# Kernel optimization log

Hardware: AMD Instinct MI355X
Metric: run time of the kernel (lower is better)

The kernel has to match this reference:

```python
import jax, jax.numpy as jnp
import numpy as np

T = 48  # top-T from init

def setup_inputs() -> dict:
    key = jax.random.key(0)
    ks = jax.random.split(key, 8)
    B, C, H, W = 16, 512, 32, 32
    tc = C // 8
    return {
        "x": jax.random.normal(ks[0], (B, C, H, W), jnp.float32),
        "fW": jax.random.normal(ks[1], (tc, C), jnp.float32) * 0.05,
        "fb": jax.random.normal(ks[2], (tc,), jnp.float32) * 0.05,
        "gW": jax.random.normal(ks[3], (tc, C), jnp.float32) * 0.05,
        "gb": jax.random.normal(ks[4], (tc,), jnp.float32) * 0.05,
        "hW": jax.random.normal(ks[5], (C, C), jnp.float32) * 0.05,
        "hb": jax.random.normal(ks[6], (C,), jnp.float32) * 0.05,
        "scale": jax.random.normal(ks[7], (1,), jnp.float32),
    }

def reference(x, fW, fb, gW, gb, hW, hb, scale):
    B, C, H, W = x.shape
    tc = fW.shape[0]
    HW = H * W
    # normalize by Frobenius norm over (batch, channel) -> [H, W]
    xn = x / jnp.linalg.norm(x, axis=(0, 1))[None, None]  # [B,C,H,W]
    # 1x1 convs, output already channel-last [B,H,W,out]
    f = jnp.einsum('bchw,oc->bhwo', xn, fW) + fb          # [B,H,W,tc]
    g = jnp.einsum('bchw,oc->bhwo', xn, gW) + gb          # [B,H,W,tc]
    h = jnp.einsum('bchw,oc->bhwo', xn, hW) + hb          # [B,H,W,C]
    xp = jnp.transpose(xn, (0, 2, 3, 1))                  # [B,H,W,C]
    # scores: queries H-major, keys W-major (faithful to permute(0,3,2,1).reshape)
    g_keys = jnp.transpose(g, (0, 3, 2, 1)).reshape(B, tc, HW)  # [B,tc,W*H]
    s = jnp.matmul(f.reshape(B, HW, tc), g_keys)          # [B,HW,HW]
    beta = jax.nn.softmax(s, axis=-1)
    o = jnp.matmul(beta, h.reshape(B, HW, C)).reshape(B, H, W, C)
    fdd = scale * o + xp                                  # [B,H,W,C]
    # per-batch correlation: fdd[b] ([H,W,C]) @ fdd[b].reshape(C,HW)
    corr = jnp.einsum('bhwc,bcn->bhwn', fdd, fdd.reshape(B, C, HW))  # [B,H,W,HW]
    top = jax.lax.top_k(corr, T)[0]                       # descending top-T values
    top = jax.nn.relu(top)
    top = top / jnp.linalg.norm(top, axis=(0, 1))[None, None]  # norm over (B,H) -> [W,T]
    return jnp.transpose(top, (0, 3, 1, 2))               # [B,T,H,W]
```

## Files before the change

### kernel.cpp

```cpp
#include <hip/hip_runtime.h>
#include <cstdint>
#include <cstddef>

#define B_   16
#define C_   512
#define H_   32
#define W_   32
#define HW_  1024
#define TC_  64
#define T_   48

typedef unsigned short u16;
typedef __attribute__((ext_vector_type(8))) short short8v;
typedef __attribute__((ext_vector_type(4))) float f32x4;

__device__ __forceinline__ u16 tobf(float x) {
    unsigned u = __float_as_uint(x);
    return (u16)((u + 0x7FFFu + ((u >> 16) & 1u)) >> 16);
}
__device__ __forceinline__ float frombf(u16 h) {
    return __uint_as_float(((unsigned)h) << 16);
}

__device__ __forceinline__ void gld16(const void* g, void* l) {
    __builtin_amdgcn_global_load_lds(
        (const __attribute__((address_space(1))) void*)g,
        (__attribute__((address_space(3))) void*)l, 16, 0, 0);
}

__global__ void k_colsq(const float* __restrict__ x, float* __restrict__ partial) {
    int bid = blockIdx.x;
    int col = (bid & 3) * 256 + threadIdx.x;
    int r0  = (bid >> 2) * 256;
    const float* p = x + (size_t)r0 * HW_ + col;
    float s = 0.f;
    for (int r = 0; r < 256; ++r) { float v = p[(size_t)r * HW_]; s += v * v; }
    partial[(size_t)(bid >> 2) * HW_ + col] = s;
}

__global__ void k_rsqrt(const float* __restrict__ partial, float* __restrict__ ninv) {
    int i = blockIdx.x * 256 + threadIdx.x;
    if (i < HW_) {
        float s = 0.f;
        for (int r = 0; r < 32; ++r) s += partial[(size_t)r * HW_ + i];
        ninv[i] = rsqrtf(s);
    }
}

__global__ void k_transpose(const float* __restrict__ x, const float* __restrict__ ninv,
                            u16* __restrict__ obH) {
    __shared__ float tile[32][33];
    int b  = blockIdx.z;
    int m0 = blockIdx.x * 32, c0 = blockIdx.y * 32;
    int tx = threadIdx.x, ty = threadIdx.y;
    const float* xb = x + (size_t)b * C_ * HW_;
    #pragma unroll
    for (int j = 0; j < 32; j += 8)
        tile[ty + j][tx] = xb[(size_t)(c0 + ty + j) * HW_ + m0 + tx];
    __syncthreads();
    size_t base = (size_t)b * HW_ * C_;
    #pragma unroll
    for (int j = 0; j < 32; j += 8) {
        int m = m0 + ty + j;
        obH[base + (size_t)m * C_ + c0 + tx] = tobf(tile[tx][ty + j] * ninv[m]);
    }
}

__global__ void k_packW(const float* __restrict__ in, u16* __restrict__ oh) {
    size_t i = (size_t)blockIdx.x * 256 + threadIdx.x;
    oh[i] = tobf(in[i]);
}
__global__ void k_packFG(const float* __restrict__ fW, const float* __restrict__ gW,
                         const float* __restrict__ fb, const float* __restrict__ gb,
                         u16* __restrict__ oh, float* __restrict__ fgb) {
    int idx = blockIdx.x * 256 + threadIdx.x;
    int row = idx >> 9, c = idx & 511;
    float v = (row < 64) ? fW[row * 512 + c] : gW[(row - 64) * 512 + c];
    oh[idx] = tobf(v);
    if (idx < 128) fgb[idx] = (idx < 64) ? fb[idx] : gb[idx - 64];
}

template<int PERMB, int EPI, int KU>
__global__ __launch_bounds__(256) void k_gemm1(
    const u16* __restrict__ A, const u16* __restrict__ Bm,
    const float* __restrict__ bias,
    float* __restrict__ Cf, u16* __restrict__ Ch,
    const float* __restrict__ scaleP,
    int N, int K, int lda, int ldb, long sA, long sB, long sC)
{
    __shared__ u16 lds[8192 * KU];
    const int b = blockIdx.z;
    const u16* pA = A + (size_t)b * sA;
    const u16* pB = Bm + (size_t)b * sB;
    const int m0 = blockIdx.y * 128, n0 = blockIdx.x * 128;
    const int tid = threadIdx.x, wave = tid >> 6, lane = tid & 63;
    const int wm = wave >> 1, wn = wave & 1;
    const int g = lane >> 4;

    f32x4 acc[4][4];
    #pragma unroll
    for (int i = 0; i < 4; ++i)
        #pragma unroll
        for (int j = 0; j < 4; ++j) { f32x4 z = {0.f,0.f,0.f,0.f}; acc[i][j] = z; }

    for (int kt = 0; kt < (K >> 5); kt += KU) {
        __syncthreads();
        #pragma unroll
        for (int u = 0; u < KU; ++u) {
            const int k0 = (kt + u) << 5;
            u16* lb = lds + u * 8192;
            #pragma unroll
            for (int q = 0; q < 4; ++q) {
                int ci = wave * 4 + q;
                bool isA = ci < 8;
                int li = ci & 7;
                const u16* gp = isA ? pA : pB;
                int ld = isA ? lda : ldb;
                int rb = isA ? m0 : n0;
                int rp = li * 8 + (lane >> 3);
                int gg = (lane & 7) ^ (rp & 7);
                int r  = rp * 2 + (gg >> 2);
                int kc = k0 + (gg & 3) * 8;
                int rowg = rb + r;
                if (PERMB && !isA) rowg = ((rowg & 31) << 5) | (rowg >> 5);
                gld16(gp + (size_t)rowg * ld + kc,
                      lb + (isA ? 0 : 4096) + li * 512 + lane * 8);
            }
        }
        __syncthreads();
        #pragma unroll
        for (int u = 0; u < KU; ++u) {
            const u16* As = lds + u * 8192;
            const u16* Bs = As + 4096;
            short8v av[4];
            #pragma unroll
            for (int i = 0; i < 4; ++i) {
                int r = wm * 64 + i * 16 + (lane & 15);
                int rp = r >> 1, gg = ((r & 1) << 2) + g;
                av[i] = *(const short8v*)(As + rp * 64 + ((gg ^ (rp & 7)) << 3));
            }
            #pragma unroll
            for (int j = 0; j < 4; ++j) {
                int r = wn * 64 + j * 16 + (lane & 15);
                int rp = r >> 1, gg = ((r & 1) << 2) + g;
                short8v bv = *(const short8v*)(Bs + rp * 64 + ((gg ^ (rp & 7)) << 3));
                #pragma unroll
                for (int i = 0; i < 4; ++i)
                    acc[i][j] = __builtin_amdgcn_mfma_f32_16x16x32_bf16(av[i], bv, acc[i][j], 0, 0, 0);
            }
        }
    }

    const float sc = (EPI == 2) ? scaleP[0] : 0.f;
    const int colbase = n0 + wn * 64 + (lane & 15);
    const int rowbase = m0 + wm * 64 + ((lane >> 4) << 2);
    #pragma unroll
    for (int i = 0; i < 4; ++i)
        #pragma unroll
        for (int j = 0; j < 4; ++j) {
            int col = colbase + j * 16;
            #pragma unroll
            for (int rg = 0; rg < 4; ++rg) {
                int row = rowbase + i * 16 + rg;
                size_t idx = (size_t)b * sC + (size_t)row * N + col;
                float a = acc[i][j][rg];
                if (EPI == 0)      Cf[idx] = a;
                else if (EPI == 2) Ch[idx] = tobf(sc * a + frombf(Ch[idx]));
                else if (EPI == 4) Ch[idx] = tobf(a);
                else if (EPI == 5) Ch[idx] = tobf(a + bias[row]);
                else               Ch[idx] = tobf(a + bias[col]);
            }
        }
}

template<int PERMB, int EPI, int KU>
__global__ __launch_bounds__(512) void k_gemm2(
    const u16* __restrict__ A, const u16* __restrict__ Bm,
    const float* __restrict__ bias,
    float* __restrict__ Cf, u16* __restrict__ Ch,
    const float* __restrict__ scaleP,
    int N, int K, int lda, int ldb, long sA, long sB, long sC)
{
    __shared__ u16 lds[12288 * KU];
    const int b = blockIdx.z;
    const u16* pA = A + (size_t)b * sA;
    const u16* pB = Bm + (size_t)b * sB;
    const int m0 = blockIdx.y * 128, n0 = blockIdx.x * 256;
    const int tid = threadIdx.x, wave = tid >> 6, lane = tid & 63;
    const int wm = wave >> 2, wn = wave & 3;
    const int g = lane >> 4;

    f32x4 acc[4][4];
    #pragma unroll
    for (int i = 0; i < 4; ++i)
        #pragma unroll
        for (int j = 0; j < 4; ++j) { f32x4 z = {0.f,0.f,0.f,0.f}; acc[i][j] = z; }

    for (int kt = 0; kt < (K >> 5); kt += KU) {
        __syncthreads();
        #pragma unroll
        for (int u = 0; u < KU; ++u) {
            const int k0 = (kt + u) << 5;
            u16* lb = lds + u * 12288;
            #pragma unroll
            for (int q = 0; q < 3; ++q) {
                int ci = wave * 3 + q;
                bool isA = ci < 8;
                int li = isA ? ci : ci - 8;
                const u16* gp = isA ? pA : pB;
                int ld = isA ? lda : ldb;
                int rb = isA ? m0 : n0;
                int rp = li * 8 + (lane >> 3);
                int gg = (lane & 7) ^ (rp & 7);
                int r  = rp * 2 + (gg >> 2);
                int kc = k0 + (gg & 3) * 8;
                int rowg = rb + r;
                if (PERMB && !isA) rowg = ((rowg & 31) << 5) | (rowg >> 5);
                gld16(gp + (size_t)rowg * ld + kc,
                      lb + (isA ? 0 : 4096) + li * 512 + lane * 8);
            }
        }
        __syncthreads();
        #pragma unroll
        for (int u = 0; u < KU; ++u) {
            const u16* As = lds + u * 12288;
            const u16* Bs = As + 4096;
            short8v av[4];
            #pragma unroll
            for (int i = 0; i < 4; ++i) {
                int r = wm * 64 + i * 16 + (lane & 15);
                int rp = r >> 1, gg = ((r & 1) << 2) + g;
                av[i] = *(const short8v*)(As + rp * 64 + ((gg ^ (rp & 7)) << 3));
            }
            #pragma unroll
            for (int j = 0; j < 4; ++j) {
                int r = wn * 64 + j * 16 + (lane & 15);
                int rp = r >> 1, gg = ((r & 1) << 2) + g;
                short8v bv = *(const short8v*)(Bs + rp * 64 + ((gg ^ (rp & 7)) << 3));
                #pragma unroll
                for (int i = 0; i < 4; ++i)
                    acc[i][j] = __builtin_amdgcn_mfma_f32_16x16x32_bf16(av[i], bv, acc[i][j], 0, 0, 0);
            }
        }
    }

    const float sc = (EPI == 2) ? scaleP[0] : 0.f;
    const int colbase = n0 + wn * 64 + (lane & 15);
    const int rowbase = m0 + wm * 64 + ((lane >> 4) << 2);
    #pragma unroll
    for (int i = 0; i < 4; ++i)
        #pragma unroll
        for (int j = 0; j < 4; ++j) {
            int col = colbase + j * 16;
            #pragma unroll
            for (int rg = 0; rg < 4; ++rg) {
                int row = rowbase + i * 16 + rg;
                size_t idx = (size_t)b * sC + (size_t)row * N + col;
                float a = acc[i][j][rg];
                if (EPI == 0)      Cf[idx] = a;
                else if (EPI == 2) Ch[idx] = tobf(sc * a + frombf(Ch[idx]));
                else if (EPI == 4) Ch[idx] = tobf(a);
                else if (EPI == 5) Ch[idx] = tobf(a + bias[row]);
                else               Ch[idx] = tobf(a + bias[col]);
            }
        }
}

__global__ __launch_bounds__(256) void k_softmax(u16* __restrict__ S) {
    size_t row = blockIdx.x;
    u16* r = S + row * (size_t)HW_;
    int t = threadIdx.x;
    ushort4 raw = ((const ushort4*)r)[t];
    float v0 = frombf(raw.x), v1 = frombf(raw.y), v2 = frombf(raw.z), v3 = frombf(raw.w);

    __shared__ float redm[4], reds[4];
    int wid = t >> 6, lane = t & 63;

    float m = fmaxf(fmaxf(v0, v1), fmaxf(v2, v3));
    for (int o = 32; o > 0; o >>= 1) m = fmaxf(m, __shfl_down(m, o));
    if (lane == 0) redm[wid] = m;
    __syncthreads();
    if (t == 0) redm[0] = fmaxf(fmaxf(redm[0], redm[1]), fmaxf(redm[2], redm[3]));
    __syncthreads();
    m = redm[0];

    v0 = expf(v0 - m); v1 = expf(v1 - m); v2 = expf(v2 - m); v3 = expf(v3 - m);
    float s = v0 + v1 + v2 + v3;
    for (int o = 32; o > 0; o >>= 1) s += __shfl_down(s, o);
    if (lane == 0) reds[wid] = s;
    __syncthreads();
    if (t == 0) reds[0] = reds[0] + reds[1] + reds[2] + reds[3];
    __syncthreads();
    float inv = 1.f / reds[0];
    ushort4 o4;
    o4.x = tobf(v0 * inv); o4.y = tobf(v1 * inv);
    o4.z = tobf(v2 * inv); o4.w = tobf(v3 * inv);
    ((ushort4*)r)[t] = o4;
}

__global__ void k_tposeU1(const u16* __restrict__ src, u16* __restrict__ dst) {
    __shared__ u16 tile[32][33];
    int b = blockIdx.z;
    const u16* sb = src + (size_t)b * (C_ * HW_);
    u16* db = dst + (size_t)b * (C_ * HW_);
    int c0 = blockIdx.x * 32, r0 = blockIdx.y * 32;
    int tx = threadIdx.x, ty = threadIdx.y;
    #pragma unroll
    for (int j = 0; j < 32; j += 8)
        tile[ty + j][tx] = sb[(size_t)(r0 + ty + j) * HW_ + c0 + tx];
    __syncthreads();
    #pragma unroll
    for (int j = 0; j < 32; j += 8)
        db[(size_t)(c0 + ty + j) * C_ + r0 + tx] = tile[tx][ty + j];
}

__device__ __forceinline__ float sort64_desc(float v, int lane) {
    #pragma unroll
    for (int k = 2; k <= 64; k <<= 1) {
        #pragma unroll
        for (int j = k >> 1; j > 0; j >>= 1) {
            float o = __shfl_xor(v, j);
            bool takeMax = (((lane & k) == 0) == ((lane & j) == 0));
            v = takeMax ? fmaxf(v, o) : fminf(v, o);
        }
    }
    return v;
}
__device__ __forceinline__ float bmerge64_desc(float a, float b, int lane) {
    float br = __shfl(b, 63 - lane);
    float c = fmaxf(a, br);
    #pragma unroll
    for (int j = 32; j > 0; j >>= 1) {
        float o = __shfl_xor(c, j);
        c = ((lane & j) == 0) ? fmaxf(c, o) : fminf(c, o);
    }
    return c;
}

__global__ __launch_bounds__(256) void k_topk(const float* __restrict__ corr,
                                              float* __restrict__ topv) {
    __shared__ float buf[4][1024];
    int wave = threadIdx.x >> 6, lane = threadIdx.x & 63;
    int row = blockIdx.x * 4 + wave;
    const float4* rp = (const float4*)(corr + (size_t)row * HW_);

    float4 e[4];
    #pragma unroll
    for (int q = 0; q < 4; ++q) e[q] = rp[lane * 4 + q];

    float gm = -INFINITY;
    #pragma unroll
    for (int q = 0; q < 4; ++q)
        gm = fmaxf(gm, fmaxf(fmaxf(e[q].x, e[q].y), fmaxf(e[q].z, e[q].w)));
    float sorted = sort64_desc(gm, lane);
    float tau = __shfl(sorted, T_ - 1);

    int c = 0;
    #pragma unroll
    for (int q = 0; q < 4; ++q)
        c += (e[q].x >= tau) + (e[q].y >= tau) + (e[q].z >= tau) + (e[q].w >= tau);
    int sc = c;
    #pragma unroll
    for (int o = 1; o < 64; o <<= 1) {
        int t2 = __shfl_up(sc, o);
        if (lane >= o) sc += t2;
    }
    int off = sc - c;
    int cnt = __shfl(sc, 63);

    float* wb = buf[wave];
    #pragma unroll
    for (int q = 0; q < 4; ++q) {
        if (e[q].x >= tau) wb[off++] = e[q].x;
        if (e[q].y >= tau) wb[off++] = e[q].y;
        if (e[q].z >= tau) wb[off++] = e[q].z;
        if (e[q].w >= tau) wb[off++] = e[q].w;
    }

    float* orow = topv + (size_t)row * T_;
    if (cnt <= 64) {
        float a = (lane < cnt) ? wb[lane] : -INFINITY;
        a = sort64_desc(a, lane);
        if (lane < T_) orow[lane] = fmaxf(a, 0.f);
    } else if (cnt <= 128) {
        float a  = sort64_desc(wb[lane], lane);
        float b2 = sort64_desc((lane < cnt - 64) ? wb[64 + lane] : -INFINITY, lane);
        float m2 = bmerge64_desc(a, b2, lane);
        if (lane < T_) orow[lane] = fmaxf(m2, 0.f);
    } else {
        int P = 256; while (P < cnt) P <<= 1;
        for (int i = cnt + lane; i < P; i += 64) wb[i] = -INFINITY;
        for (int k = 2; k <= P; k <<= 1)
            for (int j = k >> 1; j > 0; j >>= 1)
                for (int t2 = lane; t2 < P; t2 += 64) {
                    int ixj = t2 ^ j;
                    if (ixj > t2) {
                        float a = wb[t2], b3 = wb[ixj];
                        bool desc = ((t2 & k) == 0);
                        if (desc ? (a < b3) : (a > b3)) { wb[t2] = b3; wb[ixj] = a; }
                    }
                }
        if (lane < T_) orow[lane] = fmaxf(wb[lane], 0.f);
    }
}

__global__ void k_colss(const float* __restrict__ topv, float* __restrict__ colss) {
    int o = blockIdx.x;
    int w = o / T_, t = o % T_;
    int lane = threadIdx.x;
    float s = 0.f;
    for (int i = lane; i < 512; i += 64) {
        int b = i >> 5, h = i & 31;
        float v = topv[(size_t)((b << 10) + (h << 5) + w) * T_ + t];
        s += v * v;
    }
    for (int off = 32; off > 0; off >>= 1) s += __shfl_down(s, off);
    if (lane == 0) colss[o] = s;
}

__global__ void k_final(const float* __restrict__ topv, const float* __restrict__ colss,
                        float* __restrict__ out) {
    int idx = blockIdx.x * 256 + threadIdx.x;
    if (idx >= B_ * T_ * HW_) return;
    int w = idx & 31;
    int h = (idx >> 5) & 31;
    int t = (idx >> 10) % T_;
    int b = idx / (T_ * HW_);
    float v = topv[(size_t)((b << 10) + (h << 5) + w) * T_ + t];
    out[idx] = v * rsqrtf(colss[w * T_ + t]);
}

extern "C" void kernel_launch(void* const* d_in, const int* in_sizes, int n_in,
                              void* d_out, int out_size, void* d_ws, size_t ws_size,
                              hipStream_t stream) {
    const float* x     = (const float*)d_in[0];
    const float* fW    = (const float*)d_in[1];
    const float* fb    = (const float*)d_in[2];
    const float* gW    = (const float*)d_in[3];
    const float* gb    = (const float*)d_in[4];
    const float* hW    = (const float*)d_in[5];
    const float* hb    = (const float*)d_in[6];
    const float* scale = (const float*)d_in[7];
    float* out = (float*)d_out;

    char* wsb = (char*)d_ws;
    float* part = (float*)(wsb + 0);
    float* ninv = (float*)(wsb + 131072);
    u16*   hWh  = (u16*)(wsb + 135168);
    u16*   fgWh = (u16*)(wsb + 1183744);
    float* fgb  = (float*)(wsb + 1445888);
    u16*   xnH  = (u16*)(wsb + 1446400);
    u16*   fgH  = (u16*)(wsb + 35000832);
    u16*   fgL  = (u16*)(wsb + 39195136);
    u16*   hvTH = (u16*)(wsb + 43389440);
    float* S    = (float*)(wsb + 76943872);
    float* topv = (float*)fgH;
    float* colss= (float*)fgL;
    u16*   Sp   = (u16*)S;

    const long sXn = 524288;
    const long sFG = 131072;
    const long sS  = 1048576;

    k_colsq<<<128, 256, 0, stream>>>(x, part);
    k_rsqrt<<<4, 256, 0, stream>>>(part, ninv);

    k_transpose<<<dim3(32, 16, 16), dim3(32, 8), 0, stream>>>(x, ninv, xnH);

    k_packW<<<1024, 256, 0, stream>>>(hW, hWh);
    k_packFG<<<256, 256, 0, stream>>>(fW, gW, fb, gb, fgWh, fgb);

    k_gemm1<0, 6, 2><<<dim3(1, 8, 16), 256, 0, stream>>>(
        xnH, fgWh, fgb, nullptr, fgH, nullptr,
        128, 512, 512, 512, sXn, 0, sFG);

    k_gemm2<0, 5, 2><<<dim3(4, 4, 16), 512, 0, stream>>>(
        hWh, xnH, hb, nullptr, hvTH, nullptr,
        1024, 512, 512, 512, 0, sXn, sXn);

    k_gemm2<1, 4, 2><<<dim3(4, 8, 16), 512, 0, stream>>>(
        fgH, fgH + 64, nullptr, nullptr, Sp, nullptr,
        1024, 64, 128, 128, sFG, sFG, sS);

    k_softmax<<<B_ * HW_, 256, 0, stream>>>(Sp);

    k_gemm2<0, 2, 2><<<dim3(2, 8, 16), 512, 0, stream>>>(
        Sp, hvTH, nullptr, nullptr, xnH, scale,
        512, 1024, 1024, 1024, sS, sXn, sXn);

    k_tposeU1<<<dim3(32, 16, 16), dim3(32, 8), 0, stream>>>(xnH, hvTH);

    k_gemm2<0, 0, 2><<<dim3(4, 8, 16), 512, 0, stream>>>(
        xnH, hvTH, nullptr, S, nullptr, nullptr,
        1024, 512, 512, 512, sXn, sXn, sS);

    k_topk<<<B_ * HW_ / 4, 256, 0, stream>>>(S, topv);

    k_colss<<<W_ * T_, 64, 0, stream>>>(topv, colss);
    k_final<<<(B_ * T_ * HW_ + 255) / 256, 256, 0, stream>>>(topv, colss, out);
}
```

Measured before the change: 220.4 us.

## Double-buffer GEMM LDS tiles to overlap global loads with MFMA compute

Replaces the KU=2 unrolled load-then-compute loop in both GEMM kernels with a ping-pong LDS pipeline. The next K-tile is issued with async global-to-LDS loads while the current tile is computed, using partial vmcnt waits and raw s_barrier plus sched_barrier fences. The goal is to hide global memory latency behind MFMA work. In exchange there are two barriers per 32-wide K step instead of one per 64, and correctness depends on the hand-set vmcnt counts matching the loads issued per stage.

```diff
diff --git a/kernel.cpp b/kernel.cpp
--- a/kernel.cpp
+++ b/kernel.cpp
@@ -80,7 +80,7 @@
     if (idx < 128) fgb[idx] = (idx < 64) ? fb[idx] : gb[idx - 64];
 }
 
-template<int PERMB, int EPI, int KU>
+template<int PERMB, int EPI>
 __global__ __launch_bounds__(256) void k_gemm1(
     const u16* __restrict__ A, const u16* __restrict__ Bm,
     const float* __restrict__ bias,
@@ -88,7 +88,7 @@
     const float* __restrict__ scaleP,
     int N, int K, int lda, int ldb, long sA, long sB, long sC)
 {
-    __shared__ u16 lds[8192 * KU];
+    __shared__ u16 lds[2 * 8192];
     const int b = blockIdx.z;
     const u16* pA = A + (size_t)b * sA;
     const u16* pB = Bm + (size_t)b * sB;
@@ -103,52 +103,64 @@
         #pragma unroll
         for (int j = 0; j < 4; ++j) { f32x4 z = {0.f,0.f,0.f,0.f}; acc[i][j] = z; }
 
-    for (int kt = 0; kt < (K >> 5); kt += KU) {
-        __syncthreads();
-        #pragma unroll
-        for (int u = 0; u < KU; ++u) {
-            const int k0 = (kt + u) << 5;
-            u16* lb = lds + u * 8192;
+    auto STAGE = [&](int kt, int half) {
+        const int k0 = kt << 5;
+        u16* lb = lds + half * 8192;
+        #pragma unroll
+        for (int q = 0; q < 4; ++q) {
+            int ci = wave * 4 + q;
+            bool isA = ci < 8;
+            int li = ci & 7;
+            const u16* gp = isA ? pA : pB;
+            int ld = isA ? lda : ldb;
+            int rb = isA ? m0 : n0;
+            int rp = li * 8 + (lane >> 3);
+            int gg = (lane & 7) ^ (rp & 7);
+            int r  = rp * 2 + (gg >> 2);
+            int kc = k0 + (gg & 3) * 8;
+            int rowg = rb + r;
+            if (PERMB && !isA) rowg = ((rowg & 31) << 5) | (rowg >> 5);
+            gld16(gp + (size_t)rowg * ld + kc,
+                  lb + (isA ? 0 : 4096) + li * 512 + lane * 8);
+        }
+    };
+    auto COMPUTE = [&](int half) {
+        const u16* As = lds + half * 8192;
+        const u16* Bs = As + 4096;
+        short8v av[4];
+        #pragma unroll
+        for (int i = 0; i < 4; ++i) {
+            int r = wm * 64 + i * 16 + (lane & 15);
+            int rp = r >> 1, gg = ((r & 1) << 2) + g;
+            av[i] = *(const short8v*)(As + rp * 64 + ((gg ^ (rp & 7)) << 3));
+        }
+        #pragma unroll
+        for (int j = 0; j < 4; ++j) {
+            int r = wn * 64 + j * 16 + (lane & 15);
+            int rp = r >> 1, gg = ((r & 1) << 2) + g;
+            short8v bv = *(const short8v*)(Bs + rp * 64 + ((gg ^ (rp & 7)) << 3));
             #pragma unroll
-            for (int q = 0; q < 4; ++q) {
-                int ci = wave * 4 + q;
-                bool isA = ci < 8;
-                int li = ci & 7;
-                const u16* gp = isA ? pA : pB;
-                int ld = isA ? lda : ldb;
-                int rb = isA ? m0 : n0;
-                int rp = li * 8 + (lane >> 3);
-                int gg = (lane & 7) ^ (rp & 7);
-                int r  = rp * 2 + (gg >> 2);
-                int kc = k0 + (gg & 3) * 8;
-                int rowg = rb + r;
-                if (PERMB && !isA) rowg = ((rowg & 31) << 5) | (rowg >> 5);
-                gld16(gp + (size_t)rowg * ld + kc,
-                      lb + (isA ? 0 : 4096) + li * 512 + lane * 8);
-            }
-        }
-        __syncthreads();
-        #pragma unroll
-        for (int u = 0; u < KU; ++u) {
-            const u16* As = lds + u * 8192;
-            const u16* Bs = As + 4096;
-            short8v av[4];
-            #pragma unroll
-            for (int i = 0; i < 4; ++i) {
-                int r = wm * 64 + i * 16 + (lane & 15);
-                int rp = r >> 1, gg = ((r & 1) << 2) + g;
-                av[i] = *(const short8v*)(As + rp * 64 + ((gg ^ (rp & 7)) << 3));
-            }
-            #pragma unroll
-            for (int j = 0; j < 4; ++j) {
-                int r = wn * 64 + j * 16 + (lane & 15);
-                int rp = r >> 1, gg = ((r & 1) << 2) + g;
-                short8v bv = *(const short8v*)(Bs + rp * 64 + ((gg ^ (rp & 7)) << 3));
-                #pragma unroll
-                for (int i = 0; i < 4; ++i)
-                    acc[i][j] = __builtin_amdgcn_mfma_f32_16x16x32_bf16(av[i], bv, acc[i][j], 0, 0, 0);
-            }
-        }
+            for (int i = 0; i < 4; ++i)
+                acc[i][j] = __builtin_amdgcn_mfma_f32_16x16x32_bf16(av[i], bv, acc[i][j], 0, 0, 0);
+        }
+    };
+
+    const int nkt = K >> 5;
+    STAGE(0, 0);
+    int cur = 0;
+    for (int kt = 0; kt < nkt; ++kt) {
+        if (kt + 1 < nkt) {
+            STAGE(kt + 1, cur ^ 1);
+            asm volatile("s_waitcnt vmcnt(4)" ::: "memory");
+        } else {
+            asm volatile("s_waitcnt vmcnt(0)" ::: "memory");
+        }
+        __builtin_amdgcn_s_barrier();
+        __builtin_amdgcn_sched_barrier(0);
+        COMPUTE(cur);
+        __builtin_amdgcn_sched_barrier(0);
+        __builtin_amdgcn_s_barrier();
+        cur ^= 1;
     }
 
     const float sc = (EPI == 2) ? scaleP[0] : 0.f;
@@ -173,7 +185,7 @@
         }
 }
 
-template<int PERMB, int EPI, int KU>
+template<int PERMB, int EPI>
 __global__ __launch_bounds__(512) void k_gemm2(
     const u16* __restrict__ A, const u16* __restrict__ Bm,
     const float* __restrict__ bias,
@@ -181,7 +193,7 @@
     const float* __restrict__ scaleP,
     int N, int K, int lda, int ldb, long sA, long sB, long sC)
 {
-    __shared__ u16 lds[12288 * KU];
+    __shared__ u16 lds[2 * 12288];
     const int b = blockIdx.z;
     const u16* pA = A + (size_t)b * sA;
     const u16* pB = Bm + (size_t)b * sB;
@@ -196,52 +208,64 @@
         #pragma unroll
         for (int j = 0; j < 4; ++j) { f32x4 z = {0.f,0.f,0.f,0.f}; acc[i][j] = z; }
 
-    for (int kt = 0; kt < (K >> 5); kt += KU) {
-        __syncthreads();
-        #pragma unroll
-        for (int u = 0; u < KU; ++u) {
-            const int k0 = (kt + u) << 5;
-            u16* lb = lds + u * 12288;
+    auto STAGE = [&](int kt, int half) {
+        const int k0 = kt << 5;
+        u16* lb = lds + half * 12288;
+        #pragma unroll
+        for (int q = 0; q < 3; ++q) {
+            int ci = wave * 3 + q;
+            bool isA = ci < 8;
+            int li = isA ? ci : ci - 8;
+            const u16* gp = isA ? pA : pB;
+            int ld = isA ? lda : ldb;
+            int rb = isA ? m0 : n0;
+            int rp = li * 8 + (lane >> 3);
+            int gg = (lane & 7) ^ (rp & 7);
+            int r  = rp * 2 + (gg >> 2);
+            int kc = k0 + (gg & 3) * 8;
+            int rowg = rb + r;
+            if (PERMB && !isA) rowg = ((rowg & 31) << 5) | (rowg >> 5);
+            gld16(gp + (size_t)rowg * ld + kc,
+                  lb + (isA ? 0 : 4096) + li * 512 + lane * 8);
+        }
+    };
+    auto COMPUTE = [&](int half) {
+        const u16* As = lds + half * 12288;
+        const u16* Bs = As + 4096;
+        short8v av[4];
+        #pragma unroll
+        for (int i = 0; i < 4; ++i) {
+            int r = wm * 64 + i * 16 + (lane & 15);
+            int rp = r >> 1, gg = ((r & 1) << 2) + g;
+            av[i] = *(const short8v*)(As + rp * 64 + ((gg ^ (rp & 7)) << 3));
+        }
+        #pragma unroll
+        for (int j = 0; j < 4; ++j) {
+            int r = wn * 64 + j * 16 + (lane & 15);
+            int rp = r >> 1, gg = ((r & 1) << 2) + g;
+            short8v bv = *(const short8v*)(Bs + rp * 64 + ((gg ^ (rp & 7)) << 3));
             #pragma unroll
-            for (int q = 0; q < 3; ++q) {
-                int ci = wave * 3 + q;
-                bool isA = ci < 8;
-                int li = isA ? ci : ci - 8;
-                const u16* gp = isA ? pA : pB;
-                int ld = isA ? lda : ldb;
-                int rb = isA ? m0 : n0;
-                int rp = li * 8 + (lane >> 3);
-                int gg = (lane & 7) ^ (rp & 7);
-                int r  = rp * 2 + (gg >> 2);
-                int kc = k0 + (gg & 3) * 8;
-                int rowg = rb + r;
-                if (PERMB && !isA) rowg = ((rowg & 31) << 5) | (rowg >> 5);
-                gld16(gp + (size_t)rowg * ld + kc,
-                      lb + (isA ? 0 : 4096) + li * 512 + lane * 8);
-            }
-        }
-        __syncthreads();
-        #pragma unroll
-        for (int u = 0; u < KU; ++u) {
-            const u16* As = lds + u * 12288;
-            const u16* Bs = As + 4096;
-            short8v av[4];
-            #pragma unroll
-            for (int i = 0; i < 4; ++i) {
-                int r = wm * 64 + i * 16 + (lane & 15);
-                int rp = r >> 1, gg = ((r & 1) << 2) + g;
-                av[i] = *(const short8v*)(As + rp * 64 + ((gg ^ (rp & 7)) << 3));
-            }
-            #pragma unroll
-            for (int j = 0; j < 4; ++j) {
-                int r = wn * 64 + j * 16 + (lane & 15);
-                int rp = r >> 1, gg = ((r & 1) << 2) + g;
-                short8v bv = *(const short8v*)(Bs + rp * 64 + ((gg ^ (rp & 7)) << 3));
-                #pragma unroll
-                for (int i = 0; i < 4; ++i)
-                    acc[i][j] = __builtin_amdgcn_mfma_f32_16x16x32_bf16(av[i], bv, acc[i][j], 0, 0, 0);
-            }
-        }
+            for (int i = 0; i < 4; ++i)
+                acc[i][j] = __builtin_amdgcn_mfma_f32_16x16x32_bf16(av[i], bv, acc[i][j], 0, 0, 0);
+        }
+    };
+
+    const int nkt = K >> 5;
+    STAGE(0, 0);
+    int cur = 0;
+    for (int kt = 0; kt < nkt; ++kt) {
+        if (kt + 1 < nkt) {
+            STAGE(kt + 1, cur ^ 1);
+            asm volatile("s_waitcnt vmcnt(3)" ::: "memory");
+        } else {
+            asm volatile("s_waitcnt vmcnt(0)" ::: "memory");
+        }
+        __builtin_amdgcn_s_barrier();
+        __builtin_amdgcn_sched_barrier(0);
+        COMPUTE(cur);
+        __builtin_amdgcn_sched_barrier(0);
+        __builtin_amdgcn_s_barrier();
+        cur ^= 1;
     }
 
     const float sc = (EPI == 2) ? scaleP[0] : 0.f;
@@ -470,27 +494,27 @@
     k_packW<<<1024, 256, 0, stream>>>(hW, hWh);
     k_packFG<<<256, 256, 0, stream>>>(fW, gW, fb, gb, fgWh, fgb);
 
-    k_gemm1<0, 6, 2><<<dim3(1, 8, 16), 256, 0, stream>>>(
+    k_gemm1<0, 6><<<dim3(1, 8, 16), 256, 0, stream>>>(
         xnH, fgWh, fgb, nullptr, fgH, nullptr,
         128, 512, 512, 512, sXn, 0, sFG);
 
-    k_gemm2<0, 5, 2><<<dim3(4, 4, 16), 512, 0, stream>>>(
+    k_gemm2<0, 5><<<dim3(4, 4, 16), 512, 0, stream>>>(
         hWh, xnH, hb, nullptr, hvTH, nullptr,
         1024, 512, 512, 512, 0, sXn, sXn);
 
-    k_gemm2<1, 4, 2><<<dim3(4, 8, 16), 512, 0, stream>>>(
+    k_gemm2<1, 4><<<dim3(4, 8, 16), 512, 0, stream>>>(
         fgH, fgH + 64, nullptr, nullptr, Sp, nullptr,
         1024, 64, 128, 128, sFG, sFG, sS);
 
     k_softmax<<<B_ * HW_, 256, 0, stream>>>(Sp);
 
-    k_gemm2<0, 2, 2><<<dim3(2, 8, 16), 512, 0, stream>>>(
+    k_gemm2<0, 2><<<dim3(2, 8, 16), 512, 0, stream>>>(
         Sp, hvTH, nullptr, nullptr, xnH, scale,
         512, 1024, 1024, 1024, sS, sXn, sXn);
 
     k_tposeU1<<<dim3(32, 16, 16), dim3(32, 8), 0, stream>>>(xnH, hvTH);
 
-    k_gemm2<0, 0, 2><<<dim3(4, 8, 16), 512, 0, stream>>>(
+    k_gemm2<0, 0><<<dim3(4, 8, 16), 512, 0, stream>>>(
         xnH, hvTH, nullptr, S, nullptr, nullptr,
         1024, 512, 512, 512, sXn, sXn, sS);
 
```

Result: faster. 213.8 us (-3.0%).
